# Kernel tuning notes

Measured on AMD Instinct MI355X. Metric: run time of the kernel, lower is better.

## Reference

```python
import jax, jax.numpy as jnp
import numpy as np

I, H, O, K = 64, 512, 3, 6  # input, hidden, output classes, num heads


def setup_inputs() -> dict:
    key = jax.random.key(0)
    ks = jax.random.split(key, 8)
    B, T = 256, 512
    s = 0.05
    return {
        "x": jax.random.normal(ks[0], (B, T, I), dtype=jnp.float32),
        "W_ih": jax.random.normal(ks[1], (4 * H, I), dtype=jnp.float32) * s,
        "W_hh": jax.random.normal(ks[2], (4 * H, H), dtype=jnp.float32) * s,
        "b_ih": jax.random.normal(ks[3], (4 * H,), dtype=jnp.float32) * s,
        "b_hh": jax.random.normal(ks[4], (4 * H,), dtype=jnp.float32) * s,
        "W_heads": jax.random.normal(ks[5], (K, O, H), dtype=jnp.float32) * s,
        "b_heads": jax.random.normal(ks[6], (K, O), dtype=jnp.float32) * s,
    }


def _lstm_last_h(x, W_ih, W_hh, b_ih, b_hh):
    # x: [B, T, I]; returns final hidden state h_T: [B, H]
    B = x.shape[0]
    h0 = jnp.zeros((B, H), dtype=x.dtype)
    c0 = jnp.zeros((B, H), dtype=x.dtype)
    # precompute input projections for all timesteps: [T, B, 4H]
    x_proj = jnp.einsum('bti,gi->tbg', x, W_ih) + b_ih + b_hh

    def step(carry, xp_t):
        h, c = carry
        gates = xp_t + h @ W_hh.T  # [B, 4H]
        i_g, f_g, g_g, o_g = jnp.split(gates, 4, axis=-1)  # PyTorch gate order i,f,g,o
        i_g = jax.nn.sigmoid(i_g)
        f_g = jax.nn.sigmoid(f_g)
        g_g = jnp.tanh(g_g)
        o_g = jax.nn.sigmoid(o_g)
        c = f_g * c + i_g * g_g
        h = o_g * jnp.tanh(c)
        return (h, c), None

    (h_T, _), _ = jax.lax.scan(step, (h0, c0), x_proj)
    return h_T


def reference(x, W_ih, W_hh, b_ih, b_hh, W_heads, b_heads):
    h_T = _lstm_last_h(x, W_ih, W_hh, b_ih, b_hh)  # [B, H]
    # six parallel linear heads on last hidden state -> stacked [6, B, O]
    out = jnp.einsum('koh,bh->kbo', W_heads, h_T) + b_heads[:, None, :]
    return out
```

## Files before the change

### kernel.cpp

```cpp
#include <hip/hip_runtime.h>
#include <hip/hip_bf16.h>
#include <cstdint>

#define TSTEPS 512
#define BATCH  256
#define HID    512
#define INP    64
#define NGRP   16
#define GROWS  16
#define NSL    16
#define NWG    256
#define KTH    16
#define RING   8

typedef __attribute__((ext_vector_type(8))) short short8;
typedef __attribute__((ext_vector_type(4))) float f32x4;
typedef __attribute__((ext_vector_type(2))) float f32x2;
typedef __attribute__((ext_vector_type(2))) unsigned long long ull2;

#define HB_OFF    0
#define HT_OFF    (RING*BATCH*HID*2)
#define FLAGS_OFF (HT_OFF + BATCH*HID*4)
#define FLAGS_SZ  (NGRP*NSL*64)
#define CNT_OFF   (FLAGS_OFF + FLAGS_SZ)
#define ZERO2_SZ  (FLAGS_SZ + 64)

__device__ __forceinline__ unsigned cvtpk(float a, float b) {
    unsigned r;
    asm("v_cvt_pk_bf16_f32 %0, %1, %2" : "=v"(r) : "v"(a), "v"(b));
    return r;
}
__device__ __forceinline__ short8 pack8(float4 a0, float4 a1) {
    uint4 u = { cvtpk(a0.x, a0.y), cvtpk(a0.z, a0.w),
                cvtpk(a1.x, a1.y), cvtpk(a1.z, a1.w) };
    return __builtin_bit_cast(short8, u);
}
__device__ __forceinline__ float sigm(float x)  { return 1.0f/(1.0f + __expf(-x)); }
__device__ __forceinline__ float tanhf_(float x){ return 2.0f/(1.0f + __expf(-2.0f*x)) - 1.0f; }

__global__ void __launch_bounds__(256, 1)
lstm_persist(const float* __restrict__ x,   const float* __restrict__ Wih,
             const float* __restrict__ Whh, const float* __restrict__ bih,
             const float* __restrict__ bhh, const float* __restrict__ Whead,
             const float* __restrict__ bhead, float* __restrict__ out,
             char* __restrict__ ws)
{
    extern __shared__ char lds[];
    const int tid  = threadIdx.x;
    const int lane = tid & 63;
    const int wv   = tid >> 6;
    const int l15  = lane & 15, lq = lane >> 4;

    unsigned short* hb = (unsigned short*)(ws + HB_OFF);
    float* hT  = (float*)(ws + HT_OFF);
    unsigned* flags = (unsigned*)(ws + FLAGS_OFF);
    int* cnt   = (int*)(ws + CNT_OFF);

    int* org = (int*)(lds + 131056);
    if (tid == 0) {
        unsigned xcd;
        asm volatile("s_getreg_b32 %0, hwreg(HW_REG_XCC_ID)" : "=s"(xcd));
        xcd &= 7u;
        int slot = __hip_atomic_fetch_add(&cnt[xcd], 1, __ATOMIC_RELAXED, __HIP_MEMORY_SCOPE_AGENT) & 31;
        org[0] = (int)xcd * 2 + (slot >> 4);
        org[1] = slot & 15;
    }
    __syncthreads();
    const int g  = org[0];
    const int sl = org[1];
    const int hb8 = sl*32 + wv*8;

    short8 whh[KTH][2];
    #pragma unroll
    for (int kt = 0; kt < KTH; ++kt)
        #pragma unroll
        for (int m = 0; m < 2; ++m) {
            int grow = (l15 & 3)*HID + hb8 + 2*(l15 >> 2) + m;
            const float4* p = (const float4*)(Whh + (size_t)grow*HID + kt*32 + lq*8);
            whh[kt][m] = pack8(p[0], p[1]);
        }
    short8 wihf[2][2];
    #pragma unroll
    for (int kt = 0; kt < 2; ++kt)
        #pragma unroll
        for (int m = 0; m < 2; ++m) {
            int grow = (l15 & 3)*HID + hb8 + 2*(l15 >> 2) + m;
            const float4* p = (const float4*)(Wih + (size_t)grow*INP + kt*32 + lq*8);
            wihf[kt][m] = pack8(p[0], p[1]);
        }
    f32x4 bias[2];
    #pragma unroll
    for (int m = 0; m < 2; ++m)
        #pragma unroll
        for (int r = 0; r < 4; ++r) {
            int hc = hb8 + 2*lq + m;
            bias[m][r] = bih[r*HID + hc] + bhh[r*HID + hc];
        }

    unsigned short* hgrp = hb + (size_t)g*GROWS*HID;
    float*          hTg  = hT + (size_t)g*GROWS*HID;

    unsigned* flg  = flags + (size_t)g*NSL*16;
    unsigned* fpub = flg + sl*16;
    const unsigned* fpoll = flg + (4*wv + lq)*16;

    const int skt = tid >> 4, sr = tid & 15;
    char* swp = lds + skt*1024 + sr*16;
    const char* srp = lds + lane*16;

    const float* xrow = x + ((size_t)(g*GROWS + l15)*TSTEPS)*INP + lq*8;

    f32x2 cst = {0.f, 0.f};

    float4 xv0 = *(const float4*)(xrow);
    float4 xv1 = *(const float4*)(xrow + 4);
    float4 xv2 = *(const float4*)(xrow + 32);
    float4 xv3 = *(const float4*)(xrow + 36);

    #pragma clang loop unroll(disable)
    for (int t = 0; t < TSTEPS; ++t) {
        short8 bfx0 = pack8(xv0, xv1);
        short8 bfx1 = pack8(xv2, xv3);
        f32x4 a0 = bias[0], a1 = bias[1];
        f32x4 b0 = {0.f,0.f,0.f,0.f}, b1 = {0.f,0.f,0.f,0.f};
        a0 = __builtin_amdgcn_mfma_f32_16x16x32_bf16(wihf[0][0], bfx0, a0, 0, 0, 0);
        a1 = __builtin_amdgcn_mfma_f32_16x16x32_bf16(wihf[0][1], bfx0, a1, 0, 0, 0);
        b0 = __builtin_amdgcn_mfma_f32_16x16x32_bf16(wihf[1][0], bfx1, b0, 0, 0, 0);
        b1 = __builtin_amdgcn_mfma_f32_16x16x32_bf16(wihf[1][1], bfx1, b1, 0, 0, 0);
        __builtin_amdgcn_sched_barrier(0);

        if (t) {
            if (l15 == 0) {
                while (__hip_atomic_load(fpoll, __ATOMIC_RELAXED, __HIP_MEMORY_SCOPE_AGENT)
                       < (unsigned)t) {}
            }
            __builtin_amdgcn_sched_barrier(0);
            asm volatile("" ::: "memory");
        }

        {
            const char* gsrc = (const char*)(hgrp + (size_t)(t & (RING-1))*BATCH*HID)
                               + sr*1024 + skt*64;
            ull2 w0 = *(const ull2*)(gsrc);
            ull2 w1 = *(const ull2*)(gsrc + 16);
            ull2 w2 = *(const ull2*)(gsrc + 32);
            ull2 w3 = *(const ull2*)(gsrc + 48);
            *(ull2*)(swp      ) = w0;
            *(ull2*)(swp + 256) = w1;
            *(ull2*)(swp + 512) = w2;
            *(ull2*)(swp + 768) = w3;
        }
        __syncthreads();

        if (t + 1 < TSTEPS) {
            const float* xn = xrow + (size_t)(t+1)*INP;
            xv0 = *(const float4*)(xn);      xv1 = *(const float4*)(xn + 4);
            xv2 = *(const float4*)(xn + 32); xv3 = *(const float4*)(xn + 36);
        }

        #pragma unroll
        for (int k2 = 0; k2 < 8; ++k2) {
            short8 be = *(const short8*)(srp + (2*k2  )*1024);
            short8 bo = *(const short8*)(srp + (2*k2+1)*1024);
            a0 = __builtin_amdgcn_mfma_f32_16x16x32_bf16(whh[2*k2  ][0], be, a0, 0, 0, 0);
            a1 = __builtin_amdgcn_mfma_f32_16x16x32_bf16(whh[2*k2  ][1], be, a1, 0, 0, 0);
            b0 = __builtin_amdgcn_mfma_f32_16x16x32_bf16(whh[2*k2+1][0], bo, b0, 0, 0, 0);
            b1 = __builtin_amdgcn_mfma_f32_16x16x32_bf16(whh[2*k2+1][1], bo, b1, 0, 0, 0);
        }
        f32x4 acc0 = a0 + b0;
        f32x4 acc1 = a1 + b1;

        unsigned short* hbw = hgrp + (size_t)((t+1) & (RING-1))*BATCH*HID;
        float c0 = sigm(acc0[1])*cst[0] + sigm(acc0[0])*tanhf_(acc0[2]);
        float c1 = sigm(acc1[1])*cst[1] + sigm(acc1[0])*tanhf_(acc1[2]);
        cst[0] = c0; cst[1] = c1;
        float h0 = sigm(acc0[3])*tanhf_(c0);
        float h1 = sigm(acc1[3])*tanhf_(c1);
        const int cidx = l15*HID + hb8 + 2*lq;
        *(unsigned*)((char*)hbw + (size_t)cidx*2) = cvtpk(h0, h1);
        if (t == TSTEPS-1) {
            f32x2 hv2 = {h0, h1};
            *(f32x2*)(hTg + cidx) = hv2;
        }
        __syncthreads();
        if (tid == 0)
            __hip_atomic_store(fpub, (unsigned)(t+1),
                               __ATOMIC_RELAXED, __HIP_MEMORY_SCOPE_AGENT);
    }

    if (sl == 0) {
        {
            unsigned v;
            do {
                v = (lane < NSL)
                    ? __hip_atomic_load(flg + lane*16, __ATOMIC_RELAXED, __HIP_MEMORY_SCOPE_AGENT)
                    : (unsigned)TSTEPS;
            } while (!__all(v >= (unsigned)TSTEPS));
            asm volatile("" ::: "memory");
        }
        __syncthreads();
        {
            const float4* gp = (const float4*)((const char*)hTg + tid*128);
            float4* wp = (float4*)(lds + tid*128);
            #pragma unroll
            for (int j = 0; j < 8; ++j) wp[j] = gp[j];
        }
        __syncthreads();
        const float* hsm = (const float*)lds;
        for (int idx = tid; idx < 6*GROWS*3; idx += 256) {
            int k = idx / (GROWS*3), rem = idx % (GROWS*3);
            int row = rem / 3, o = rem % 3;
            const float* wp = Whead + ((size_t)k*3 + o)*HID;
            const float* hp = hsm + row*HID;
            float s = 0.f;
            for (int hh = 0; hh < HID; hh += 4) {
                float4 hv = *(const float4*)(hp + hh);
                float4 wv2 = *(const float4*)(wp + hh);
                s += hv.x*wv2.x + hv.y*wv2.y + hv.z*wv2.z + hv.w*wv2.w;
            }
            out[((size_t)k*BATCH + g*GROWS + row)*3 + o] = s + bhead[k*3 + o];
        }
    }
}

extern "C" void kernel_launch(void* const* d_in, const int* in_sizes, int n_in,
                              void* d_out, int out_size, void* d_ws, size_t ws_size,
                              hipStream_t stream) {
    (void)in_sizes; (void)n_in; (void)out_size; (void)ws_size;
    const float* x     = (const float*)d_in[0];
    const float* Wih   = (const float*)d_in[1];
    const float* Whh   = (const float*)d_in[2];
    const float* bih   = (const float*)d_in[3];
    const float* bhh   = (const float*)d_in[4];
    const float* Whead = (const float*)d_in[5];
    const float* bhead = (const float*)d_in[6];
    char* ws = (char*)d_ws;

    (void)hipFuncSetAttribute((const void*)lstm_persist,
                              hipFuncAttributeMaxDynamicSharedMemorySize, 131072);

    (void)hipMemsetAsync(ws + HB_OFF, 0, BATCH*HID*2, stream);
    (void)hipMemsetAsync(ws + FLAGS_OFF, 0, ZERO2_SZ, stream);

    hipLaunchKernelGGL(lstm_persist, dim3(NWG), dim3(256), 131072, stream,
                       x, Wih, Whh, bih, bhh, Whead, bhead, (float*)d_out, ws);
}
```

Measured before the change: 1.078 ms.

## Double-buffer LDS h tiles, replace end-of-step barrier with LDS counter publish

Stages the incoming h tile into alternating LDS buffers so the trailing __syncthreads can be removed. Each wave increments an LDS atomic counter after draining its global stores, and the last wave to arrive publishes the step flag. Each wave also starts its MFMA chain on its own freshly written k-tiles before the barrier, and the flag poll is issued early so the spin loop is skipped when the flag is already set. This shortens the serial per-step critical path in the recurrence, but it relies on relaxed atomics plus vmcnt waits for cross-workgroup visibility, which adds ordering risk.

```diff
diff --git a/kernel.cpp b/kernel.cpp
--- a/kernel.cpp
+++ b/kernel.cpp
@@ -55,6 +55,7 @@
     float* hT  = (float*)(ws + HT_OFF);
     unsigned* flags = (unsigned*)(ws + FLAGS_OFF);
     int* cnt   = (int*)(ws + CNT_OFF);
+    unsigned* ldscnt = (unsigned*)(lds + 32768);
 
     int* org = (int*)(lds + 131056);
     if (tid == 0) {
@@ -64,6 +65,7 @@
         int slot = __hip_atomic_fetch_add(&cnt[xcd], 1, __ATOMIC_RELAXED, __HIP_MEMORY_SCOPE_AGENT) & 31;
         org[0] = (int)xcd * 2 + (slot >> 4);
         org[1] = slot & 15;
+        *ldscnt = 0;
     }
     __syncthreads();
     const int g  = org[0];
@@ -119,6 +121,10 @@
 
     #pragma clang loop unroll(disable)
     for (int t = 0; t < TSTEPS; ++t) {
+        unsigned pf = 0xffffffffu;
+        if (t && l15 == 0)
+            pf = __hip_atomic_load(fpoll, __ATOMIC_RELAXED, __HIP_MEMORY_SCOPE_AGENT);
+
         short8 bfx0 = pack8(xv0, xv1);
         short8 bfx1 = pack8(xv2, xv3);
         f32x4 a0 = bias[0], a1 = bias[1];
@@ -130,14 +136,18 @@
         __builtin_amdgcn_sched_barrier(0);
 
         if (t) {
-            if (l15 == 0) {
-                while (__hip_atomic_load(fpoll, __ATOMIC_RELAXED, __HIP_MEMORY_SCOPE_AGENT)
-                       < (unsigned)t) {}
+            if (!__all(pf >= (unsigned)t)) {
+                if (l15 == 0) {
+                    while (__hip_atomic_load(fpoll, __ATOMIC_RELAXED, __HIP_MEMORY_SCOPE_AGENT)
+                           < (unsigned)t) {}
+                }
             }
             __builtin_amdgcn_sched_barrier(0);
             asm volatile("" ::: "memory");
         }
 
+        char* swp_t = swp + (t & 1)*16384;
+        const char* srp_t = srp + (t & 1)*16384;
         {
             const char* gsrc = (const char*)(hgrp + (size_t)(t & (RING-1))*BATCH*HID)
                                + sr*1024 + skt*64;
@@ -145,10 +155,23 @@
             ull2 w1 = *(const ull2*)(gsrc + 16);
             ull2 w2 = *(const ull2*)(gsrc + 32);
             ull2 w3 = *(const ull2*)(gsrc + 48);
-            *(ull2*)(swp      ) = w0;
-            *(ull2*)(swp + 256) = w1;
-            *(ull2*)(swp + 512) = w2;
-            *(ull2*)(swp + 768) = w3;
+            *(ull2*)(swp_t      ) = w0;
+            *(ull2*)(swp_t + 256) = w1;
+            *(ull2*)(swp_t + 512) = w2;
+            *(ull2*)(swp_t + 768) = w3;
+        }
+
+        #pragma unroll
+        for (int j = 0; j < 4; ++j) {
+            int kt = 4*wv + j;
+            short8 bf = *(const short8*)(srp_t + kt*1024);
+            if (j & 1) {
+                b0 = __builtin_amdgcn_mfma_f32_16x16x32_bf16(whh[kt][0], bf, b0, 0, 0, 0);
+                b1 = __builtin_amdgcn_mfma_f32_16x16x32_bf16(whh[kt][1], bf, b1, 0, 0, 0);
+            } else {
+                a0 = __builtin_amdgcn_mfma_f32_16x16x32_bf16(whh[kt][0], bf, a0, 0, 0, 0);
+                a1 = __builtin_amdgcn_mfma_f32_16x16x32_bf16(whh[kt][1], bf, a1, 0, 0, 0);
+            }
         }
         __syncthreads();
 
@@ -159,13 +182,16 @@
         }
 
         #pragma unroll
-        for (int k2 = 0; k2 < 8; ++k2) {
-            short8 be = *(const short8*)(srp + (2*k2  )*1024);
-            short8 bo = *(const short8*)(srp + (2*k2+1)*1024);
-            a0 = __builtin_amdgcn_mfma_f32_16x16x32_bf16(whh[2*k2  ][0], be, a0, 0, 0, 0);
-            a1 = __builtin_amdgcn_mfma_f32_16x16x32_bf16(whh[2*k2  ][1], be, a1, 0, 0, 0);
-            b0 = __builtin_amdgcn_mfma_f32_16x16x32_bf16(whh[2*k2+1][0], bo, b0, 0, 0, 0);
-            b1 = __builtin_amdgcn_mfma_f32_16x16x32_bf16(whh[2*k2+1][1], bo, b1, 0, 0, 0);
+        for (int j = 4; j < 16; ++j) {
+            int kt = (4*wv + j) & 15;
+            short8 bf = *(const short8*)(srp_t + kt*1024);
+            if (j & 1) {
+                b0 = __builtin_amdgcn_mfma_f32_16x16x32_bf16(whh[kt][0], bf, b0, 0, 0, 0);
+                b1 = __builtin_amdgcn_mfma_f32_16x16x32_bf16(whh[kt][1], bf, b1, 0, 0, 0);
+            } else {
+                a0 = __builtin_amdgcn_mfma_f32_16x16x32_bf16(whh[kt][0], bf, a0, 0, 0, 0);
+                a1 = __builtin_amdgcn_mfma_f32_16x16x32_bf16(whh[kt][1], bf, a1, 0, 0, 0);
+            }
         }
         f32x4 acc0 = a0 + b0;
         f32x4 acc1 = a1 + b1;
@@ -182,10 +208,16 @@
             f32x2 hv2 = {h0, h1};
             *(f32x2*)(hTg + cidx) = hv2;
         }
-        __syncthreads();
-        if (tid == 0)
-            __hip_atomic_store(fpub, (unsigned)(t+1),
-                               __ATOMIC_RELAXED, __HIP_MEMORY_SCOPE_AGENT);
+
+        asm volatile("s_waitcnt vmcnt(0)" ::: "memory");
+        __builtin_amdgcn_sched_barrier(0);
+        if (lane == 0) {
+            unsigned old = __hip_atomic_fetch_add(ldscnt, 1u, __ATOMIC_RELAXED,
+                                                  __HIP_MEMORY_SCOPE_WORKGROUP);
+            if (old == (unsigned)(4*t + 3))
+                __hip_atomic_store(fpub, (unsigned)(t+1),
+                                   __ATOMIC_RELAXED, __HIP_MEMORY_SCOPE_AGENT);
+        }
     }
 
     if (sl == 0) {
```

Result: slower. 3.055 ms (+183.4%).
